# Performance work log

Measured on AMD Instinct MI355X. Metric: run time of the kernel, lower is better.

The kernel has to match this reference:

```python
import jax, jax.numpy as jnp
import numpy as np
from jax import lax

N = 512       # encoder channels
B = 128       # bottleneck channels
K = 3         # depthwise kernel
NUM_BLOCKS = 8
NUM_REPEATS = 3
NUM_SPK = 2
NBLK = NUM_BLOCKS * NUM_REPEATS  # 24
DILATIONS = [2 ** i for i in range(NUM_BLOCKS)] * NUM_REPEATS
EPS = 1e-5


def setup_inputs() -> dict:
    key = jax.random.key(0)
    ks = jax.random.split(key, 12)
    b, L = 4, 8000
    x = jax.random.normal(ks[0], (b, N, L), dtype=jnp.float32)
    # outer GroupNorm affine
    gn_g = 1.0 + 0.05 * jax.random.normal(ks[1], (N,), dtype=jnp.float32)
    gn_b = 0.05 * jax.random.normal(ks[2], (N,), dtype=jnp.float32)
    # 1x1 compression N->B
    w_comp = 0.05 * jax.random.normal(ks[3], (B, N), dtype=jnp.float32)
    # per-block params stacked on leading axis
    dw_w = 0.1 * jax.random.normal(ks[4], (NBLK, B, 1, K), dtype=jnp.float32)   # depthwise weights
    pr_a = 0.25 * jnp.ones((NBLK, B), dtype=jnp.float32) + 0.01 * jax.random.normal(ks[5], (NBLK, B), dtype=jnp.float32)
    tn_g = 1.0 + 0.05 * jax.random.normal(ks[6], (NBLK, B), dtype=jnp.float32)
    tn_b = 0.05 * jax.random.normal(ks[7], (NBLK, B), dtype=jnp.float32)
    pw_w = 0.08 * jax.random.normal(ks[8], (NBLK, B, B), dtype=jnp.float32)     # pointwise 1x1
    # 1x1 expansion B -> N*num_speakers
    w_exp = 0.05 * jax.random.normal(ks[9], (N * NUM_SPK, B), dtype=jnp.float32)
    return {"x": x, "gn_g": gn_g, "gn_b": gn_b, "w_comp": w_comp,
            "dw_w": dw_w, "pr_a": pr_a, "tn_g": tn_g, "tn_b": tn_b,
            "pw_w": pw_w, "w_exp": w_exp}


def _gnorm1(h, g, b):
    # GroupNorm(1, C): normalize over (C, L) per sample, per-channel affine
    m = jnp.mean(h, axis=(1, 2), keepdims=True)
    v = jnp.mean((h - m) ** 2, axis=(1, 2), keepdims=True)
    return (h - m) * lax.rsqrt(v + EPS) * g[None, :, None] + b[None, :, None]


def reference(x, gn_g, gn_b, w_comp, dw_w, pr_a, tn_g, tn_b, pw_w, w_exp):
    out = _gnorm1(x, gn_g, gn_b)                         # [b, N, L]
    out = jnp.einsum('on,bnl->bol', w_comp, out)          # [b, B, L]
    for i in range(NBLK):
        d = DILATIONS[i]
        res = out
        pad_L = (K - 1) * d
        h = jnp.pad(out, ((0, 0), (0, 0), (pad_L, 0)))    # causal left pad
        h = lax.conv_general_dilated(
            h, dw_w[i], window_strides=(1,), padding='VALID',
            rhs_dilation=(d,), dimension_numbers=('NCH', 'OIH', 'NCH'),
            feature_group_count=B)                        # depthwise dilated conv
        a = pr_a[i][None, :, None]
        h = jnp.where(h > 0, h, a * h)                    # PReLU
        h = _gnorm1(h, tn_g[i], tn_b[i])
        h = jnp.einsum('oc,bcl->bol', pw_w[i], h)         # 1x1 pointwise
        out = h + res
    out = jnp.einsum('oc,bcl->bol', w_exp, out)           # [b, N*spk, L]
    out = jax.nn.sigmoid(out)
    b, _, L = out.shape
    return out.reshape(b, NUM_SPK, N, L)
```

## Files before the change

### kernel.cpp

```cpp
#include <hip/hip_runtime.h>
#include <hip/hip_bf16.h>
#include <math.h>
#include <cstddef>

#define LSEQ 8000
#define EPS 1e-5f

typedef unsigned short ushort_t;
typedef __attribute__((ext_vector_type(8))) short s16x8;
typedef __attribute__((ext_vector_type(4))) float f32x4;
typedef __attribute__((ext_vector_type(4))) unsigned short us16x4;

__device__ __forceinline__ ushort_t f2bf(float f) {
    union { float f; unsigned u; } x; x.f = f;
    unsigned r = x.u + 0x7FFFu + ((x.u >> 16) & 1u);
    return (ushort_t)(r >> 16);
}
__device__ __forceinline__ float bf2f(ushort_t h) {
    union { unsigned u; float f; } x; x.u = ((unsigned)h) << 16;
    return x.f;
}

__global__ void cvt_split_kernel(const float* __restrict__ src,
                                 ushort_t* __restrict__ hi, ushort_t* __restrict__ lo, int n) {
    for (int i = blockIdx.x * blockDim.x + threadIdx.x; i < n; i += gridDim.x * blockDim.x) {
        float v = src[i];
        ushort_t h = f2bf(v);
        hi[i] = h;
        lo[i] = f2bf(v - bf2f(h));
    }
}

__global__ __launch_bounds__(256)
void stats_plain(const float* __restrict__ in, int C, float* __restrict__ stats) {
    int b = blockIdx.y, c = blockIdx.x;
    const float* row = in + ((size_t)b * C + c) * LSEQ;
    float s = 0.f, sq = 0.f;
    for (int l4 = threadIdx.x * 4; l4 < LSEQ; l4 += 1024) {
        float4 v = *(const float4*)(row + l4);
        s += v.x + v.y + v.z + v.w;
        sq += v.x * v.x + v.y * v.y + v.z * v.z + v.w * v.w;
    }
    for (int off = 32; off > 0; off >>= 1) {
        s += __shfl_down(s, off, 64);
        sq += __shfl_down(sq, off, 64);
    }
    __shared__ float red[4][2];
    int wid = threadIdx.x >> 6, lane = threadIdx.x & 63;
    if (lane == 0) { red[wid][0] = s; red[wid][1] = sq; }
    __syncthreads();
    if (threadIdx.x == 0) {
        float ts = red[0][0] + red[1][0] + red[2][0] + red[3][0];
        float tq = red[0][1] + red[1][1] + red[2][1] + red[3][1];
        atomicAdd(&stats[b * 2 + 0], ts);
        atomicAdd(&stats[b * 2 + 1], tq);
    }
}

__global__ __launch_bounds__(320)
void conv_split_stats(const float* __restrict__ in,
                      const float* __restrict__ dw,
                      const float* __restrict__ pa,
                      int dil,
                      ushort_t* __restrict__ hH, ushort_t* __restrict__ hL,
                      float* __restrict__ stats)
{
    __shared__ float Ls[8][576];
    __shared__ float dwl[8][4];
    __shared__ float red[5][2];
    int tid = threadIdx.x;
    int g = blockIdx.y, b = blockIdx.z;
    int l0 = blockIdx.x * 320;
    const float* base = in + ((size_t)b * 128 + g * 8) * LSEQ;

    for (int idx = tid; idx < 8 * 144; idx += 320) {
        int r = idx / 144, f4 = idx % 144;
        int off = l0 - 256 + f4 * 4;
        const float* rp = base + (size_t)r * LSEQ;
        float4 v;
        if (off >= 0) {
            v = *(const float4*)(rp + off);
        } else {
            v.x = 0.f;
            v.y = (off + 1 >= 0) ? rp[off + 1] : 0.f;
            v.z = (off + 2 >= 0) ? rp[off + 2] : 0.f;
            v.w = (off + 3 >= 0) ? rp[off + 3] : 0.f;
        }
        *(float4*)&Ls[r][f4 * 4] = v;
    }
    if (tid < 32) {
        int j = tid >> 2, q = tid & 3;
        dwl[j][q] = (q < 3) ? dw[(g * 8 + j) * 3 + q] : pa[g * 8 + j];
    }
    __syncthreads();

    float s = 0.f, sq = 0.f;
    s16x8 hv, lv;
    int lt = tid;
#pragma unroll
    for (int j = 0; j < 8; j++) {
        float x2 = Ls[j][256 + lt];
        float x1 = Ls[j][256 + lt - dil];
        float x0 = Ls[j][256 + lt - 2 * dil];
        float h = fmaf(dwl[j][0], x0, fmaf(dwl[j][1], x1, dwl[j][2] * x2));
        h = h > 0.f ? h : dwl[j][3] * h;
        s += h; sq += h * h;
        ushort_t hb = f2bf(h);
        hv[j] = (short)hb;
        lv[j] = (short)f2bf(h - bf2f(hb));
    }
    size_t o = (((size_t)b * 16 + g) * LSEQ + l0 + lt) * 8;
    *(s16x8*)(hH + o) = hv;
    *(s16x8*)(hL + o) = lv;

    for (int off = 32; off > 0; off >>= 1) {
        s += __shfl_down(s, off, 64);
        sq += __shfl_down(sq, off, 64);
    }
    int wid = tid >> 6, lane = tid & 63;
    if (lane == 0) { red[wid][0] = s; red[wid][1] = sq; }
    __syncthreads();
    if (tid == 0) {
        float ts = 0.f, tq = 0.f;
        for (int i = 0; i < 5; i++) { ts += red[i][0]; tq += red[i][1]; }
        atomicAdd(&stats[b * 2 + 0], ts);
        atomicAdd(&stats[b * 2 + 1], tq);
    }
}

template<int KT>
__global__ __launch_bounds__(256)
void fold_kernel(const float* __restrict__ W,
                 const float* __restrict__ gam, const float* __restrict__ bet,
                 const float* __restrict__ stats,
                 float invCN,
                 ushort_t* __restrict__ WH, ushort_t* __restrict__ WL,
                 float* __restrict__ bias)
{
    int chunk = blockIdx.x, b = blockIdx.y, tid = threadIdx.x;
    float m = stats[b * 2 + 0] * invCN;
    float var = stats[b * 2 + 1] * invCN - m * m;
    float rs = rsqrtf(var + EPS);

    size_t base = (size_t)chunk * 8 * KT;
    ushort_t* WHb = WH + (size_t)b * 128 * KT;
    ushort_t* WLb = WL + (size_t)b * 128 * KT;
#pragma unroll
    for (int it = 0; it < (8 * KT) / 1024; ++it) {
        int i = it * 1024 + tid * 4;
        int c = i & (KT - 1);
        float4 w4 = *(const float4*)(W + base + i);
        float4 g4 = *(const float4*)(gam + c);
        float v0 = w4.x * g4.x * rs, v1 = w4.y * g4.y * rs;
        float v2 = w4.z * g4.z * rs, v3 = w4.w * g4.w * rs;
        us16x4 hv, lv;
        ushort_t h0 = f2bf(v0); hv[0] = h0; lv[0] = f2bf(v0 - bf2f(h0));
        ushort_t h1 = f2bf(v1); hv[1] = h1; lv[1] = f2bf(v1 - bf2f(h1));
        ushort_t h2 = f2bf(v2); hv[2] = h2; lv[2] = f2bf(v2 - bf2f(h2));
        ushort_t h3 = f2bf(v3); hv[3] = h3; lv[3] = f2bf(v3 - bf2f(h3));
        *(us16x4*)(WHb + base + i) = hv;
        *(us16x4*)(WLb + base + i) = lv;
    }

    int rg = tid >> 5;
    int lane32 = tid & 31;
    int row = chunk * 8 + rg;
    const float* wr = W + (size_t)row * KT;
    float acc = 0.f;
#pragma unroll
    for (int it = 0; it < KT / 128; ++it) {
        int c = it * 128 + lane32 * 4;
        float4 w4 = *(const float4*)(wr + c);
        float4 g4 = *(const float4*)(gam + c);
        float4 b4 = *(const float4*)(bet + c);
        acc += w4.x * (b4.x - m * rs * g4.x);
        acc += w4.y * (b4.y - m * rs * g4.y);
        acc += w4.z * (b4.z - m * rs * g4.z);
        acc += w4.w * (b4.w - m * rs * g4.w);
    }
#pragma unroll
    for (int off = 16; off > 0; off >>= 1)
        acc += __shfl_down(acc, off, 32);
    if (lane32 == 0) bias[b * 128 + row] = acc;
}

template<int KTOT, int MROWS, int OTILES, int STAGE, bool WPERB, bool BIAS, bool HASRES, bool SIG>
__global__ __launch_bounds__(256)
void gemm_mfma(const float* __restrict__ inF,
               const ushort_t* __restrict__ hH, const ushort_t* __restrict__ hL,
               const ushort_t* __restrict__ WH, const ushort_t* __restrict__ WL,
               const float* __restrict__ bias,
               const float* __restrict__ res,
               float* __restrict__ outp)
{
    constexpr int NCHUNK = KTOT / 128;
    static_assert(OTILES == 1 || NCHUNK == 1, "");
    __shared__ ushort_t hsH[16 * 64 * 8];
    __shared__ ushort_t hsL[16 * 64 * 8];

    int tid = threadIdx.x;
    int b = blockIdx.z;
    int l0 = blockIdx.x * 64;
    int wave = tid >> 6, lane = tid & 63;
    int lg = lane >> 4, lr = lane & 15;
    int rowoff = (wave >> 1) * 64, coloff = (wave & 1) * 32;

    f32x4 acc[4][2];

    for (int ot = 0; ot < OTILES; ot++) {
#pragma unroll
        for (int rf = 0; rf < 4; rf++)
#pragma unroll
            for (int cf = 0; cf < 2; cf++)
                acc[rf][cf] = (f32x4){0.f, 0.f, 0.f, 0.f};

        for (int kc = 0; kc < NCHUNK; kc++) {
            if (ot == 0) {
                __syncthreads();
                if constexpr (STAGE == 0) {
                    int scol = lane;
#pragma unroll
                    for (int gi = 0; gi < 4; gi++) {
                        int g = wave * 4 + gi;
                        size_t src = (((size_t)b * 16 + g) * LSEQ + l0 + scol) * 8;
                        s16x8 hv = *(const s16x8*)(hH + src);
                        s16x8 lv = *(const s16x8*)(hL + src);
                        int slot = (g * 64 + (scol ^ ((g & 3) << 1))) * 8;
                        *(s16x8*)&hsH[slot] = hv;
                        *(s16x8*)&hsL[slot] = lv;
                    }
                } else {
                    int scol = tid & 63;
                    int sg0 = (tid >> 6) * 4;
#pragma unroll
                    for (int gi = 0; gi < 4; gi++) {
                        int gk = sg0 + gi;
                        s16x8 hv, lv;
#pragma unroll
                        for (int j = 0; j < 8; j++) {
                            int c = kc * 128 + gk * 8 + j;
                            float v = inF[((size_t)b * KTOT + c) * LSEQ + l0 + scol];
                            ushort_t hb = f2bf(v);
                            hv[j] = (short)hb;
                            lv[j] = (short)f2bf(v - bf2f(hb));
                        }
                        int slot = (gk * 64 + (scol ^ ((gk & 3) << 1))) * 8;
                        *(s16x8*)&hsH[slot] = hv;
                        *(s16x8*)&hsL[slot] = lv;
                    }
                }
                __syncthreads();
            }

#pragma unroll
            for (int ks = 0; ks < 4; ks++) {
                s16x8 aH[4], aL[4];
#pragma unroll
                for (int rf = 0; rf < 4; rf++) {
                    int row = ot * 128 + rowoff + rf * 16 + lr;
                    size_t woff = ((size_t)(WPERB ? b : 0) * MROWS + row) * KTOT
                                  + kc * 128 + ks * 32 + lg * 8;
                    aH[rf] = *(const s16x8*)(WH + woff);
                    aL[rf] = *(const s16x8*)(WL + woff);
                }
#pragma unroll
                for (int cf = 0; cf < 2; cf++) {
                    int col = coloff + cf * 16 + lr;
                    int gk = ks * 4 + lg;
                    int slot = (gk * 64 + (col ^ ((gk & 3) << 1))) * 8;
                    s16x8 bH = *(const s16x8*)&hsH[slot];
                    s16x8 bL = *(const s16x8*)&hsL[slot];
#pragma unroll
                    for (int rf = 0; rf < 4; rf++) {
                        acc[rf][cf] = __builtin_amdgcn_mfma_f32_16x16x32_bf16(aH[rf], bH, acc[rf][cf], 0, 0, 0);
                        acc[rf][cf] = __builtin_amdgcn_mfma_f32_16x16x32_bf16(aH[rf], bL, acc[rf][cf], 0, 0, 0);
                        acc[rf][cf] = __builtin_amdgcn_mfma_f32_16x16x32_bf16(aL[rf], bH, acc[rf][cf], 0, 0, 0);
                    }
                }
            }
        }

#pragma unroll
        for (int rf = 0; rf < 4; rf++) {
#pragma unroll
            for (int cf = 0; cf < 2; cf++) {
#pragma unroll
                for (int r = 0; r < 4; r++) {
                    int rloc = rowoff + rf * 16 + lg * 4 + r;
                    int row = ot * 128 + rloc;
                    int col = l0 + coloff + cf * 16 + lr;
                    size_t idx = ((size_t)b * MROWS + row) * LSEQ + col;
                    float v = acc[rf][cf][r];
                    if (BIAS) v += bias[b * 128 + rloc];
                    if (HASRES) v += res[idx];
                    if (SIG) v = 1.f / (1.f + __expf(-v));
                    outp[idx] = v;
                }
            }
        }
    }
}

extern "C" void kernel_launch(void* const* d_in, const int* in_sizes, int n_in,
                              void* d_out, int out_size, void* d_ws, size_t ws_size,
                              hipStream_t stream) {
    const float* x      = (const float*)d_in[0];
    const float* gn_g   = (const float*)d_in[1];
    const float* gn_b   = (const float*)d_in[2];
    const float* w_comp = (const float*)d_in[3];
    const float* dw_w   = (const float*)d_in[4];
    const float* pr_a   = (const float*)d_in[5];
    const float* tn_g   = (const float*)d_in[6];
    const float* tn_b   = (const float*)d_in[7];
    const float* pw_w   = (const float*)d_in[8];
    const float* w_exp  = (const float*)d_in[9];
    float* out = (float*)d_out;

    const size_t ACTF = (size_t)4 * 128 * LSEQ;
    float* bufA = (float*)d_ws;
    float* bufB = bufA + ACTF;
    ushort_t* hH   = (ushort_t*)(bufB + ACTF);
    ushort_t* hL   = hH + ACTF;
    ushort_t* wcFH = hL + ACTF;
    ushort_t* wcFL = wcFH + (size_t)4 * 128 * 512;
    ushort_t* wfH  = wcFL + (size_t)4 * 128 * 512;
    ushort_t* wfL  = wfH + (size_t)4 * 128 * 128;
    ushort_t* weH  = wfL + (size_t)4 * 128 * 128;
    ushort_t* weL  = weH + (size_t)1024 * 128;
    float* biasF = (float*)(weL + (size_t)1024 * 128);
    float* biasM = biasF + 512;
    float* stats = biasM + 512;

    hipMemsetAsync(stats, 0, 25 * 4 * 2 * sizeof(float), stream);

    cvt_split_kernel<<<dim3(256), 256, 0, stream>>>(w_exp, weH, weL, 1024 * 128);

    stats_plain<<<dim3(512, 4), 256, 0, stream>>>(x, 512, stats);
    fold_kernel<512><<<dim3(16, 4), 256, 0, stream>>>(
        w_comp, gn_g, gn_b, stats, 1.f / (512.f * (float)LSEQ), wcFH, wcFL, biasF);
    gemm_mfma<512, 128, 1, 1, true, true, false, false><<<dim3(125, 1, 4), 256, 0, stream>>>(
        x, nullptr, nullptr, wcFH, wcFL, biasF, nullptr, bufA);

    float* cur = bufA;
    float* nxt = bufB;
    for (int i = 0; i < 24; i++) {
        int dil = 1 << (i & 7);
        float* st = stats + (size_t)(1 + i) * 8;
        conv_split_stats<<<dim3(25, 16, 4), 320, 0, stream>>>(
            cur, dw_w + (size_t)i * 384, pr_a + (size_t)i * 128, dil, hH, hL, st);
        fold_kernel<128><<<dim3(16, 4), 256, 0, stream>>>(
            pw_w + (size_t)i * 16384, tn_g + (size_t)i * 128, tn_b + (size_t)i * 128,
            st, 1.f / (128.f * (float)LSEQ), wfH, wfL, biasM);
        gemm_mfma<128, 128, 1, 0, true, true, true, false><<<dim3(125, 1, 4), 256, 0, stream>>>(
            nullptr, hH, hL, wfH, wfL, biasM, cur, nxt);
        float* tmp = cur; cur = nxt; nxt = tmp;
    }

    gemm_mfma<128, 1024, 8, 1, false, false, false, true><<<dim3(125, 1, 4), 256, 0, stream>>>(
        cur, nullptr, nullptr, weH, weL, nullptr, nullptr, out);
}
```

Measured before the change: 1.906 ms.

## Use 512-thread GEMM blocks and spread expansion output tiles across grid

The MFMA GEMM kernel now runs 8 waves per block, each owning a 64x16 output tile instead of 4 waves with 64x32 tiles, which halves per-wave accumulator and B-fragment work. The final expansion GEMM no longer loops over 8 output tiles inside one block; the tiles move to blockIdx.y, giving 8x more blocks. The intent is more parallelism and latency hiding. In exchange, the expansion stage re-stages and re-splits the same input activations to bf16 in every output-tile block, and each wave reuses fewer weight fragments per column.

Result: slower. 2.163 ms (+13.5%).

```diff
diff --git a/kernel.cpp b/kernel.cpp
--- a/kernel.cpp
+++ b/kernel.cpp
@@ -184,8 +184,8 @@
     if (lane32 == 0) bias[b * 128 + row] = acc;
 }
 
-template<int KTOT, int MROWS, int OTILES, int STAGE, bool WPERB, bool BIAS, bool HASRES, bool SIG>
-__global__ __launch_bounds__(256)
+template<int KTOT, int MROWS, int STAGE, bool WPERB, bool BIAS, bool HASRES, bool SIG>
+__global__ __launch_bounds__(512)
 void gemm_mfma(const float* __restrict__ inF,
                const ushort_t* __restrict__ hH, const ushort_t* __restrict__ hL,
                const ushort_t* __restrict__ WH, const ushort_t* __restrict__ WL,
@@ -194,109 +194,95 @@
                float* __restrict__ outp)
 {
     constexpr int NCHUNK = KTOT / 128;
-    static_assert(OTILES == 1 || NCHUNK == 1, "");
     __shared__ ushort_t hsH[16 * 64 * 8];
     __shared__ ushort_t hsL[16 * 64 * 8];
 
     int tid = threadIdx.x;
     int b = blockIdx.z;
     int l0 = blockIdx.x * 64;
+    int obase = blockIdx.y * 128;
     int wave = tid >> 6, lane = tid & 63;
     int lg = lane >> 4, lr = lane & 15;
-    int rowoff = (wave >> 1) * 64, coloff = (wave & 1) * 32;
-
-    f32x4 acc[4][2];
-
-    for (int ot = 0; ot < OTILES; ot++) {
-#pragma unroll
-        for (int rf = 0; rf < 4; rf++)
-#pragma unroll
-            for (int cf = 0; cf < 2; cf++)
-                acc[rf][cf] = (f32x4){0.f, 0.f, 0.f, 0.f};
-
-        for (int kc = 0; kc < NCHUNK; kc++) {
-            if (ot == 0) {
-                __syncthreads();
-                if constexpr (STAGE == 0) {
-                    int scol = lane;
-#pragma unroll
-                    for (int gi = 0; gi < 4; gi++) {
-                        int g = wave * 4 + gi;
-                        size_t src = (((size_t)b * 16 + g) * LSEQ + l0 + scol) * 8;
-                        s16x8 hv = *(const s16x8*)(hH + src);
-                        s16x8 lv = *(const s16x8*)(hL + src);
-                        int slot = (g * 64 + (scol ^ ((g & 3) << 1))) * 8;
-                        *(s16x8*)&hsH[slot] = hv;
-                        *(s16x8*)&hsL[slot] = lv;
-                    }
-                } else {
-                    int scol = tid & 63;
-                    int sg0 = (tid >> 6) * 4;
-#pragma unroll
-                    for (int gi = 0; gi < 4; gi++) {
-                        int gk = sg0 + gi;
-                        s16x8 hv, lv;
-#pragma unroll
-                        for (int j = 0; j < 8; j++) {
-                            int c = kc * 128 + gk * 8 + j;
-                            float v = inF[((size_t)b * KTOT + c) * LSEQ + l0 + scol];
-                            ushort_t hb = f2bf(v);
-                            hv[j] = (short)hb;
-                            lv[j] = (short)f2bf(v - bf2f(hb));
-                        }
-                        int slot = (gk * 64 + (scol ^ ((gk & 3) << 1))) * 8;
-                        *(s16x8*)&hsH[slot] = hv;
-                        *(s16x8*)&hsL[slot] = lv;
-                    }
+    int rowoff = (wave >> 2) * 64;
+    int coloff = (wave & 3) * 16;
+
+    f32x4 acc[4];
+#pragma unroll
+    for (int rf = 0; rf < 4; rf++) acc[rf] = (f32x4){0.f, 0.f, 0.f, 0.f};
+
+    for (int kc = 0; kc < NCHUNK; kc++) {
+        __syncthreads();
+        if constexpr (STAGE == 0) {
+            int scol = lane;
+#pragma unroll
+            for (int gi = 0; gi < 2; gi++) {
+                int g = wave * 2 + gi;
+                size_t src = (((size_t)b * 16 + g) * LSEQ + l0 + scol) * 8;
+                s16x8 hv = *(const s16x8*)(hH + src);
+                s16x8 lv = *(const s16x8*)(hL + src);
+                int slot = (g * 64 + (scol ^ ((g & 3) << 1))) * 8;
+                *(s16x8*)&hsH[slot] = hv;
+                *(s16x8*)&hsL[slot] = lv;
+            }
+        } else {
+            int scol = lane;
+#pragma unroll
+            for (int gi = 0; gi < 2; gi++) {
+                int gk = wave * 2 + gi;
+                s16x8 hv, lv;
+#pragma unroll
+                for (int j = 0; j < 8; j++) {
+                    int c = kc * 128 + gk * 8 + j;
+                    float v = inF[((size_t)b * KTOT + c) * LSEQ + l0 + scol];
+                    ushort_t hb = f2bf(v);
+                    hv[j] = (short)hb;
+                    lv[j] = (short)f2bf(v - bf2f(hb));
                 }
-                __syncthreads();
-            }
-
-#pragma unroll
-            for (int ks = 0; ks < 4; ks++) {
-                s16x8 aH[4], aL[4];
-#pragma unroll
-                for (int rf = 0; rf < 4; rf++) {
-                    int row = ot * 128 + rowoff + rf * 16 + lr;
-                    size_t woff = ((size_t)(WPERB ? b : 0) * MROWS + row) * KTOT
-                                  + kc * 128 + ks * 32 + lg * 8;
-                    aH[rf] = *(const s16x8*)(WH + woff);
-                    aL[rf] = *(const s16x8*)(WL + woff);
-                }
-#pragma unroll
-                for (int cf = 0; cf < 2; cf++) {
-                    int col = coloff + cf * 16 + lr;
-                    int gk = ks * 4 + lg;
-                    int slot = (gk * 64 + (col ^ ((gk & 3) << 1))) * 8;
-                    s16x8 bH = *(const s16x8*)&hsH[slot];
-                    s16x8 bL = *(const s16x8*)&hsL[slot];
-#pragma unroll
-                    for (int rf = 0; rf < 4; rf++) {
-                        acc[rf][cf] = __builtin_amdgcn_mfma_f32_16x16x32_bf16(aH[rf], bH, acc[rf][cf], 0, 0, 0);
-                        acc[rf][cf] = __builtin_amdgcn_mfma_f32_16x16x32_bf16(aH[rf], bL, acc[rf][cf], 0, 0, 0);
-                        acc[rf][cf] = __builtin_amdgcn_mfma_f32_16x16x32_bf16(aL[rf], bH, acc[rf][cf], 0, 0, 0);
-                    }
-                }
+                int slot = (gk * 64 + (scol ^ ((gk & 3) << 1))) * 8;
+                *(s16x8*)&hsH[slot] = hv;
+                *(s16x8*)&hsL[slot] = lv;
             }
         }
-
-#pragma unroll
-        for (int rf = 0; rf < 4; rf++) {
-#pragma unroll
-            for (int cf = 0; cf < 2; cf++) {
-#pragma unroll
-                for (int r = 0; r < 4; r++) {
-                    int rloc = rowoff + rf * 16 + lg * 4 + r;
-                    int row = ot * 128 + rloc;
-                    int col = l0 + coloff + cf * 16 + lr;
-                    size_t idx = ((size_t)b * MROWS + row) * LSEQ + col;
-                    float v = acc[rf][cf][r];
-                    if (BIAS) v += bias[b * 128 + rloc];
-                    if (HASRES) v += res[idx];
-                    if (SIG) v = 1.f / (1.f + __expf(-v));
-                    outp[idx] = v;
-                }
+        __syncthreads();
+
+#pragma unroll
+        for (int ks = 0; ks < 4; ks++) {
+            s16x8 aH[4], aL[4];
+#pragma unroll
+            for (int rf = 0; rf < 4; rf++) {
+                int row = obase + rowoff + rf * 16 + lr;
+                size_t woff = ((size_t)(WPERB ? b : 0) * MROWS + row) * KTOT
+                              + kc * 128 + ks * 32 + lg * 8;
+                aH[rf] = *(const s16x8*)(WH + woff);
+                aL[rf] = *(const s16x8*)(WL + woff);
             }
+            int col = coloff + lr;
+            int gk = ks * 4 + lg;
+            int slot = (gk * 64 + (col ^ ((gk & 3) << 1))) * 8;
+            s16x8 bH = *(const s16x8*)&hsH[slot];
+            s16x8 bL = *(const s16x8*)&hsL[slot];
+#pragma unroll
+            for (int rf = 0; rf < 4; rf++) {
+                acc[rf] = __builtin_amdgcn_mfma_f32_16x16x32_bf16(aH[rf], bH, acc[rf], 0, 0, 0);
+                acc[rf] = __builtin_amdgcn_mfma_f32_16x16x32_bf16(aH[rf], bL, acc[rf], 0, 0, 0);
+                acc[rf] = __builtin_amdgcn_mfma_f32_16x16x32_bf16(aL[rf], bH, acc[rf], 0, 0, 0);
+            }
+        }
+    }
+
+#pragma unroll
+    for (int rf = 0; rf < 4; rf++) {
+#pragma unroll
+        for (int r = 0; r < 4; r++) {
+            int rloc = rowoff + rf * 16 + lg * 4 + r;
+            int row = obase + rloc;
+            int col = l0 + coloff + lr;
+            size_t idx = ((size_t)b * MROWS + row) * LSEQ + col;
+            float v = acc[rf][r];
+            if (BIAS) v += bias[b * 128 + rloc];
+            if (HASRES) v += res[idx];
+            if (SIG) v = 1.f / (1.f + __expf(-v));
+            outp[idx] = v;
         }
     }
 }
@@ -338,7 +324,7 @@
     stats_plain<<<dim3(512, 4), 256, 0, stream>>>(x, 512, stats);
     fold_kernel<512><<<dim3(16, 4), 256, 0, stream>>>(
         w_comp, gn_g, gn_b, stats, 1.f / (512.f * (float)LSEQ), wcFH, wcFL, biasF);
-    gemm_mfma<512, 128, 1, 1, true, true, false, false><<<dim3(125, 1, 4), 256, 0, stream>>>(
+    gemm_mfma<512, 128, 1, true, true, false, false><<<dim3(125, 1, 4), 512, 0, stream>>>(
         x, nullptr, nullptr, wcFH, wcFL, biasF, nullptr, bufA);
 
     float* cur = bufA;
@@ -351,11 +337,11 @@
         fold_kernel<128><<<dim3(16, 4), 256, 0, stream>>>(
             pw_w + (size_t)i * 16384, tn_g + (size_t)i * 128, tn_b + (size_t)i * 128,
             st, 1.f / (128.f * (float)LSEQ), wfH, wfL, biasM);
-        gemm_mfma<128, 128, 1, 0, true, true, true, false><<<dim3(125, 1, 4), 256, 0, stream>>>(
+        gemm_mfma<128, 128, 0, true, true, true, false><<<dim3(125, 1, 4), 512, 0, stream>>>(
             nullptr, hH, hL, wfH, wfL, biasM, cur, nxt);
         float* tmp = cur; cur = nxt; nxt = tmp;
     }
 
-    gemm_mfma<128, 1024, 8, 1, false, false, false, true><<<dim3(125, 1, 4), 256, 0, stream>>>(
+    gemm_mfma<128, 1024, 1, false, false, false, true><<<dim3(125, 8, 4), 512, 0, stream>>>(
         cur, nullptr, nullptr, weH, weL, nullptr, nullptr, out);
 }
```
